# Optimization experiments

Hardware: AMD Instinct MI355X
Metric: run time of the kernel (lower is better)

The kernel has to match this reference:

```python
import jax, jax.numpy as jnp
import numpy as np

NUM_CODEBOOKS = 2
CODEBOOK_SIZE = 256
OUT_GROUP = 1
IN_GROUP = 8
IN_FEATURES = 4096
OUT_FEATURES = 11008


def setup_inputs() -> dict:
    key = jax.random.key(0)
    k1, k2, k3, k4, k5 = jax.random.split(key, 5)
    num_out_groups = OUT_FEATURES // OUT_GROUP
    num_in_groups = IN_FEATURES // IN_GROUP
    x = jax.random.normal(k1, (4, 2048, IN_FEATURES), dtype=jnp.float32)
    codes = jax.random.randint(k2, (num_out_groups, num_in_groups, NUM_CODEBOOKS), 0, CODEBOOK_SIZE, dtype=jnp.int32)
    codebooks = jax.random.normal(k3, (NUM_CODEBOOKS, CODEBOOK_SIZE, OUT_GROUP, IN_GROUP), dtype=jnp.float32) * 0.05
    scales = jax.random.uniform(k4, (num_out_groups, 1, 1, 1), dtype=jnp.float32)
    bias = jax.random.normal(k5, (OUT_FEATURES,), dtype=jnp.float32)
    return {"x": x, "codes": codes, "codebooks": codebooks, "scales": scales, "bias": bias}


def _dequantize_weight(codes, codebooks, scales):
    # codes: [Og, Ig, C] int; codebooks: [C, K, og, ig]; scales: [Og,1,1,1]
    C = codebooks.shape[0]
    og, ig = codebooks.shape[2], codebooks.shape[3]
    Og, Ig = codes.shape[0], codes.shape[1]
    # gather per-codebook vectors: result [Og, Ig, C, og, ig]
    w = codebooks[jnp.arange(C)[None, None, :], codes]
    w = w.sum(axis=2)                      # [Og, Ig, og, ig] (additive quantization)
    w = w * scales                         # broadcast [Og,1,1,1]
    w = w.transpose(0, 2, 1, 3)            # [Og, og, Ig, ig]
    return w.reshape(Og * og, Ig * ig)     # [out_features, in_features]


def reference(x, codes, codebooks, scales, bias):
    W = _dequantize_weight(codes, codebooks, scales)
    return jnp.einsum('bsi,oi->bso', x, W) + bias
```

## Files before the change

kernel.cpp:

```cpp
#include <hip/hip_runtime.h>
#include <hip/hip_bf16.h>
#include <stdint.h>

#define IN_F 4096
#define OUT_F 11008
#define M_ROWS 8192
#define NIG 512
#define CBSZ 256

typedef _Float16 f16x8 __attribute__((ext_vector_type(8)));
typedef float f32x4 __attribute__((ext_vector_type(4)));

__global__ __launch_bounds__(256) void dequant_w_kernel(
    const int* __restrict__ codes, const float* __restrict__ cbs,
    _Float16* __restrict__ W)
{
  const int idx = blockIdx.x * 256 + threadIdx.x;
  const int2 c = ((const int2*)codes)[idx];
  const float4* e0 = (const float4*)(cbs + (size_t)c.x * 8);
  const float4* e1 = (const float4*)(cbs + (size_t)CBSZ * 8 + (size_t)c.y * 8);
  const float4 a0 = e0[0], a1 = e0[1];
  const float4 b0 = e1[0], b1 = e1[1];
  f16x8 w;
  w[0] = (_Float16)(a0.x + b0.x);
  w[1] = (_Float16)(a0.y + b0.y);
  w[2] = (_Float16)(a0.z + b0.z);
  w[3] = (_Float16)(a0.w + b0.w);
  w[4] = (_Float16)(a1.x + b1.x);
  w[5] = (_Float16)(a1.y + b1.y);
  w[6] = (_Float16)(a1.z + b1.z);
  w[7] = (_Float16)(a1.w + b1.w);
  *(f16x8*)(W + (size_t)idx * 8) = w;
}

__global__ __launch_bounds__(256) void convert_x_kernel(
    const float* __restrict__ x, _Float16* __restrict__ X)
{
  const size_t i = ((size_t)blockIdx.x * 256 + threadIdx.x) * 8;
  const float4 a = *(const float4*)(x + i);
  const float4 b = *(const float4*)(x + i + 4);
  f16x8 v;
  v[0] = (_Float16)a.x; v[1] = (_Float16)a.y;
  v[2] = (_Float16)a.z; v[3] = (_Float16)a.w;
  v[4] = (_Float16)b.x; v[5] = (_Float16)b.y;
  v[6] = (_Float16)b.z; v[7] = (_Float16)b.w;
  *(f16x8*)(X + i) = v;
}

#define BM 256
#define BN 256
#define BK 64
#define NKT (IN_F / BK)
#define GRID_MT (M_ROWS / BM)
#define GRID_NT (OUT_F / BN)

__global__ __launch_bounds__(512, 2) void gemm_pipe(
    const _Float16* __restrict__ X, const _Float16* __restrict__ Wd,
    const float* __restrict__ scales, const float* __restrict__ bias,
    float* __restrict__ out)
{
  __shared__ char smem[131072];

  const int cpx = (GRID_MT * GRID_NT) >> 3;
  const int wg = (blockIdx.x & 7) * cpx + (blockIdx.x >> 3);
  const int mt = wg & (GRID_MT - 1), nt = wg >> 5;
  const int m0 = mt * BM, n0 = nt * BN;

  const int t_ = threadIdx.x;
  const int wave = t_ >> 6, lane = t_ & 63;
  const int wm = wave >> 2, wn = wave & 3;
  const int r16 = lane & 15;
  const int q = lane >> 4;
  const int sw = r16 & 7;
  const int c0 = ((q ^ sw) << 4);
  const int c1 = (((4 | q) ^ sw) << 4);

  const int s_row0 = t_ >> 3;
  const int s_col  = (((t_ & 7) ^ ((t_ >> 3) & 7)) << 3);
  const _Float16* asrc = X  + (size_t)(m0 + s_row0) * IN_F + s_col;
  const _Float16* bsrc = Wd + (size_t)(n0 + s_row0) * IN_F + s_col;
  const int s_dst = wave * 1024;

  f32x4 acc[8][4] = {};
  f16x8 al0[4], al1[4], ah0[4], ah1[4], bl0[2], bl1[2], bh0[2], bh1[2];

#define GLD(gsrc, ldst) __builtin_amdgcn_global_load_lds(                     \
    (const __attribute__((address_space(1))) void*)(gsrc),                    \
    (__attribute__((address_space(3))) void*)(ldst), 16, 0, 0)
#define STAGE_A(kt, bufc, i) GLD(asrc + (size_t)(kt) * BK + (size_t)(i) * 64 * IN_F, \
    smem + (bufc) * 65536 + (i) * 8192 + s_dst)
#define STAGE_B(kt, bufc, i) GLD(bsrc + (size_t)(kt) * BK + (size_t)(i) * 64 * IN_F, \
    smem + (bufc) * 65536 + 32768 + (i) * 8192 + s_dst)

#define RD_A(bufp, mm, cc) (*(const f16x8*)((bufp) + ((wm * 128 + (mm) * 16 + r16) << 7) + (cc)))
#define RD_B(bufp, nn, cc) (*(const f16x8*)((bufp) + 32768 + ((wn * 64 + (nn) * 16 + r16) << 7) + (cc)))

#define BAR   __builtin_amdgcn_s_barrier()
#define PRIO1 __builtin_amdgcn_s_setprio(1)
#define PRIO0 __builtin_amdgcn_s_setprio(0)
#define VM4 asm volatile("s_waitcnt vmcnt(4)" ::: "memory")
#define VM2 asm volatile("s_waitcnt vmcnt(2)" ::: "memory")
#define VM0 asm volatile("s_waitcnt vmcnt(0)" ::: "memory")

#define MG(AF, BF, MO, NO)                                                    \
    _Pragma("unroll")                                                         \
    for (int m = 0; m < 4; ++m)                                               \
      _Pragma("unroll")                                                       \
      for (int n = 0; n < 2; ++n)                                             \
        acc[(MO) + m][(NO) + n] = __builtin_amdgcn_mfma_f32_16x16x32_f16(     \
            AF[m], BF[n], acc[(MO) + m][(NO) + n], 0, 0, 0)

#define TILE(P, tt, STG, G2, G4) do {                                         \
    const char* bufT = smem + (P) * 65536;                                    \
                           \
    if (STG) { STAGE_A((tt) + 1, 1 - (P), 0); STAGE_A((tt) + 1, 1 - (P), 2); }\
    _Pragma("unroll")                                                         \
    for (int m = 0; m < 4; ++m) { al0[m] = RD_A(bufT, m, c0);                 \
                                  al1[m] = RD_A(bufT, m, c1); }               \
    _Pragma("unroll")                                                         \
    for (int n = 0; n < 2; ++n) { bl0[n] = RD_B(bufT, n, c0);                 \
                                  bl1[n] = RD_B(bufT, n, c1); }               \
    BAR; PRIO1; MG(al0, bl0, 0, 0); MG(al1, bl1, 0, 0); PRIO0; BAR;           \
                        \
    if (STG) { STAGE_B((tt) + 1, 1 - (P), 0); STAGE_B((tt) + 1, 1 - (P), 1); }\
    _Pragma("unroll")                                                         \
    for (int n = 0; n < 2; ++n) { bh0[n] = RD_B(bufT, 2 + n, c0);             \
                                  bh1[n] = RD_B(bufT, 2 + n, c1); }           \
    BAR; PRIO1; MG(al0, bh0, 0, 2); MG(al1, bh1, 0, 2); PRIO0;                \
    if ((G2) == 4) { VM4; }                                                   \
    if ((G2) == 0) { VM0; }                                                   \
    BAR;                                                                      \
                              \
    if (STG) { STAGE_B((tt) + 1, 1 - (P), 2); STAGE_B((tt) + 1, 1 - (P), 3); }\
    _Pragma("unroll")                                                         \
    for (int m = 0; m < 4; ++m) { ah0[m] = RD_A(bufT, 4 + m, c0);             \
                                  ah1[m] = RD_A(bufT, 4 + m, c1); }           \
    BAR; PRIO1; MG(ah0, bh0, 4, 2); MG(ah1, bh1, 4, 2); PRIO0; BAR;           \
                        \
    if (STG) { STAGE_A((tt) + 1, 1 - (P), 1); STAGE_A((tt) + 1, 1 - (P), 3); }\
    PRIO1; MG(ah0, bl0, 4, 0); MG(ah1, bl1, 4, 0); PRIO0;                     \
    if ((G4) == 2) { VM2; }                                                   \
    BAR;                                                                      \
  } while (0)

  STAGE_A(0, 0, 0); STAGE_A(0, 0, 2);
  STAGE_B(0, 0, 0); STAGE_B(0, 0, 1);
  STAGE_B(0, 0, 2); STAGE_B(0, 0, 3);
  STAGE_A(0, 0, 1); STAGE_A(0, 0, 3);
  VM2;
  BAR;

  #pragma unroll 1
  for (int t = 0; t < 62; t += 2) {
    TILE(0, t,     1, 4, 2);
    TILE(1, t + 1, 1, 4, 2);
  }
  TILE(0, 62, 1, 4, 2);
  TILE(1, 63, 0, 0, -1);

  const int crow = (lane >> 4) << 2;
  #pragma unroll
  for (int nf = 0; nf < 4; ++nf) {
    const int col = n0 + wn * 64 + nf * 16 + r16;
    const float s = scales[col];
    const float bb = bias[col];
    #pragma unroll
    for (int mf = 0; mf < 8; ++mf) {
      const int rb = m0 + wm * 128 + mf * 16 + crow;
      #pragma unroll
      for (int r = 0; r < 4; ++r)
        out[(size_t)(rb + r) * OUT_F + col] = acc[mf][nf][r] * s + bb;
    }
  }
#undef TILE
#undef MG
#undef RD_A
#undef RD_B
#undef STAGE_A
#undef STAGE_B
#undef GLD
}

__global__ __launch_bounds__(256) void naive_kernel(
    const float* __restrict__ x, const int* __restrict__ codes,
    const float* __restrict__ cbs, const float* __restrict__ scales,
    const float* __restrict__ bias, float* __restrict__ out)
{
  __shared__ float xrow[IN_F];
  const int m = blockIdx.x;
  for (int i = threadIdx.x; i < IN_F; i += 256)
    xrow[i] = x[(size_t)m * IN_F + i];
  __syncthreads();
  for (int o = threadIdx.x; o < OUT_F; o += 256) {
    float acc = 0.f;
    const int2* crow = (const int2*)codes + (size_t)o * NIG;
    for (int g = 0; g < NIG; ++g) {
      const int2 c = crow[g];
      const float* e0 = cbs + (size_t)c.x * 8;
      const float* e1 = cbs + (size_t)CBSZ * 8 + (size_t)c.y * 8;
      const float* xr = xrow + g * 8;
      #pragma unroll
      for (int j = 0; j < 8; ++j) acc += (e0[j] + e1[j]) * xr[j];
    }
    out[(size_t)m * OUT_F + o] = acc * scales[o] + bias[o];
  }
}

extern "C" void kernel_launch(void* const* d_in, const int* in_sizes, int n_in,
                              void* d_out, int out_size, void* d_ws, size_t ws_size,
                              hipStream_t stream) {
  const float* x      = (const float*)d_in[0];
  const int*   codes  = (const int*)d_in[1];
  const float* cbs    = (const float*)d_in[2];
  const float* scales = (const float*)d_in[3];
  const float* bias   = (const float*)d_in[4];
  float* out = (float*)d_out;

  const size_t W_BYTES = (size_t)OUT_F * IN_F * sizeof(_Float16);
  const size_t X_BYTES = (size_t)M_ROWS * IN_F * sizeof(_Float16);

  if (ws_size < W_BYTES + X_BYTES) {
    naive_kernel<<<M_ROWS, 256, 0, stream>>>(x, codes, cbs, scales, bias, out);
    return;
  }

  _Float16* W = (_Float16*)d_ws;
  _Float16* X = (_Float16*)((char*)d_ws + W_BYTES);

  dequant_w_kernel<<<(OUT_F * NIG) / 256, 256, 0, stream>>>(codes, cbs, W);
  convert_x_kernel<<<(M_ROWS * IN_F / 8) / 256, 256, 0, stream>>>(x, X);
  gemm_pipe<<<GRID_MT * GRID_NT, 512, 0, stream>>>(X, W, scales, bias, out);
}
```

Before: 818.0 us.

## Issue all next-tile loads up front and cut per-tile barriers to one

Restructures the double-buffered GEMM main loop so that all eight global-to-LDS loads for the next K tile are issued at the start of each tile, instead of being spread across four phases. The LDS reads and MFMAs are regrouped by K half (c0, then c1), and sched_barrier fences replace most workgroup barriers, leaving a single vmcnt(0) wait plus one barrier per tile. This is meant to cut barrier and synchronisation overhead and let MFMA issue run longer without stalls. In exchange, each tile ends with a full wait on outstanding loads, which removes the partial-wait overlap the old vmcnt(4)/vmcnt(2) schedule had and may expose load latency.

```diff
diff --git a/kernel.cpp b/kernel.cpp
--- a/kernel.cpp
+++ b/kernel.cpp
@@ -98,8 +98,7 @@
 #define BAR   __builtin_amdgcn_s_barrier()
 #define PRIO1 __builtin_amdgcn_s_setprio(1)
 #define PRIO0 __builtin_amdgcn_s_setprio(0)
-#define VM4 asm volatile("s_waitcnt vmcnt(4)" ::: "memory")
-#define VM2 asm volatile("s_waitcnt vmcnt(2)" ::: "memory")
+#define SBAR0 __builtin_amdgcn_sched_barrier(0)
 #define VM0 asm volatile("s_waitcnt vmcnt(0)" ::: "memory")
 
 #define MG(AF, BF, MO, NO)                                                    \
@@ -110,53 +109,58 @@
         acc[(MO) + m][(NO) + n] = __builtin_amdgcn_mfma_f32_16x16x32_f16(     \
             AF[m], BF[n], acc[(MO) + m][(NO) + n], 0, 0, 0)
 
-#define TILE(P, tt, STG, G2, G4) do {                                         \
+#define TILE(P, tt, STG, GATE) do {                                           \
     const char* bufT = smem + (P) * 65536;                                    \
-                           \
-    if (STG) { STAGE_A((tt) + 1, 1 - (P), 0); STAGE_A((tt) + 1, 1 - (P), 2); }\
-    _Pragma("unroll")                                                         \
-    for (int m = 0; m < 4; ++m) { al0[m] = RD_A(bufT, m, c0);                 \
-                                  al1[m] = RD_A(bufT, m, c1); }               \
+    if (STG) {                                                                \
+      STAGE_A((tt) + 1, 1 - (P), 0); STAGE_A((tt) + 1, 1 - (P), 1);           \
+      STAGE_A((tt) + 1, 1 - (P), 2); STAGE_A((tt) + 1, 1 - (P), 3);           \
+      STAGE_B((tt) + 1, 1 - (P), 0); STAGE_B((tt) + 1, 1 - (P), 1);           \
+      STAGE_B((tt) + 1, 1 - (P), 2); STAGE_B((tt) + 1, 1 - (P), 3);           \
+    }                                                                         \
+    SBAR0;                                                                    \
+         \
+    _Pragma("unroll")                                                         \
+    for (int m = 0; m < 4; ++m) al0[m] = RD_A(bufT, m, c0);                   \
     _Pragma("unroll")                                                         \
     for (int n = 0; n < 2; ++n) { bl0[n] = RD_B(bufT, n, c0);                 \
-                                  bl1[n] = RD_B(bufT, n, c1); }               \
-    BAR; PRIO1; MG(al0, bl0, 0, 0); MG(al1, bl1, 0, 0); PRIO0; BAR;           \
-                        \
-    if (STG) { STAGE_B((tt) + 1, 1 - (P), 0); STAGE_B((tt) + 1, 1 - (P), 1); }\
-    _Pragma("unroll")                                                         \
-    for (int n = 0; n < 2; ++n) { bh0[n] = RD_B(bufT, 2 + n, c0);             \
+                                  bh0[n] = RD_B(bufT, 2 + n, c0); }           \
+    _Pragma("unroll")                                                         \
+    for (int m = 0; m < 4; ++m) ah0[m] = RD_A(bufT, 4 + m, c0);               \
+    SBAR0;                                                                    \
+    PRIO1;                                                                    \
+    MG(al0, bl0, 0, 0); MG(al0, bh0, 0, 2);                                   \
+    MG(ah0, bh0, 4, 2); MG(ah0, bl0, 4, 0);                                   \
+    PRIO0;                                                                    \
+    SBAR0;                                                                    \
+                                                           \
+    _Pragma("unroll")                                                         \
+    for (int m = 0; m < 4; ++m) al1[m] = RD_A(bufT, m, c1);                   \
+    _Pragma("unroll")                                                         \
+    for (int n = 0; n < 2; ++n) { bl1[n] = RD_B(bufT, n, c1);                 \
                                   bh1[n] = RD_B(bufT, 2 + n, c1); }           \
-    BAR; PRIO1; MG(al0, bh0, 0, 2); MG(al1, bh1, 0, 2); PRIO0;                \
-    if ((G2) == 4) { VM4; }                                                   \
-    if ((G2) == 0) { VM0; }                                                   \
-    BAR;                                                                      \
-                              \
-    if (STG) { STAGE_B((tt) + 1, 1 - (P), 2); STAGE_B((tt) + 1, 1 - (P), 3); }\
-    _Pragma("unroll")                                                         \
-    for (int m = 0; m < 4; ++m) { ah0[m] = RD_A(bufT, 4 + m, c0);             \
-                                  ah1[m] = RD_A(bufT, 4 + m, c1); }           \
-    BAR; PRIO1; MG(ah0, bh0, 4, 2); MG(ah1, bh1, 4, 2); PRIO0; BAR;           \
-                        \
-    if (STG) { STAGE_A((tt) + 1, 1 - (P), 1); STAGE_A((tt) + 1, 1 - (P), 3); }\
-    PRIO1; MG(ah0, bl0, 4, 0); MG(ah1, bl1, 4, 0); PRIO0;                     \
-    if ((G4) == 2) { VM2; }                                                   \
-    BAR;                                                                      \
+    _Pragma("unroll")                                                         \
+    for (int m = 0; m < 4; ++m) ah1[m] = RD_A(bufT, 4 + m, c1);               \
+    SBAR0;                                                                    \
+    PRIO1;                                                                    \
+    MG(al1, bl1, 0, 0); MG(al1, bh1, 0, 2);                                   \
+    MG(ah1, bh1, 4, 2); MG(ah1, bl1, 4, 0);                                   \
+    PRIO0;                                                                    \
+    SBAR0;                                                                    \
+    if (GATE) { VM0; BAR; }       \
   } while (0)
 
-  STAGE_A(0, 0, 0); STAGE_A(0, 0, 2);
-  STAGE_B(0, 0, 0); STAGE_B(0, 0, 1);
-  STAGE_B(0, 0, 2); STAGE_B(0, 0, 3);
-  STAGE_A(0, 0, 1); STAGE_A(0, 0, 3);
-  VM2;
+  STAGE_A(0, 0, 0); STAGE_A(0, 0, 1); STAGE_A(0, 0, 2); STAGE_A(0, 0, 3);
+  STAGE_B(0, 0, 0); STAGE_B(0, 0, 1); STAGE_B(0, 0, 2); STAGE_B(0, 0, 3);
+  VM0;
   BAR;
 
   #pragma unroll 1
   for (int t = 0; t < 62; t += 2) {
-    TILE(0, t,     1, 4, 2);
-    TILE(1, t + 1, 1, 4, 2);
-  }
-  TILE(0, 62, 1, 4, 2);
-  TILE(1, 63, 0, 0, -1);
+    TILE(0, t,     1, 1);
+    TILE(1, t + 1, 1, 1);
+  }
+  TILE(0, 62, 1, 1);
+  TILE(1, 63, 0, 0);
 
   const int crow = (lane >> 4) << 2;
   #pragma unroll
```

Result: slower. 854.8 us (+4.5%).

## Load B operand straight from global into registers and drop its LDS staging

Applied to the files above, without the earlier changes.

The GEMM no longer stages the dequantized weight tile (B) through shared memory. Each wave now loads its B fragments directly from global memory into registers, prefetching the next k-tile's low half one tile ahead. Only the activation tile (A) stays double-buffered in LDS, which halves the LDS footprint. Most intra-tile workgroup barriers become scheduling barriers, with a single vmcnt wait plus barrier per tile. The aim is to cut LDS traffic and barrier stalls, at the cost of duplicated B global/L2 reads across the two M-waves and exposed global-load latency in registers.

```diff
diff --git a/kernel.cpp b/kernel.cpp
--- a/kernel.cpp
+++ b/kernel.cpp
@@ -59,7 +59,7 @@
     const float* __restrict__ scales, const float* __restrict__ bias,
     float* __restrict__ out)
 {
-  __shared__ char smem[131072];
+  __shared__ char smem[65536];
 
   const int cpx = (GRID_MT * GRID_NT) >> 3;
   const int wg = (blockIdx.x & 7) * cpx + (blockIdx.x >> 3);
@@ -77,30 +77,30 @@
 
   const int s_row0 = t_ >> 3;
   const int s_col  = (((t_ & 7) ^ ((t_ >> 3) & 7)) << 3);
-  const _Float16* asrc = X  + (size_t)(m0 + s_row0) * IN_F + s_col;
-  const _Float16* bsrc = Wd + (size_t)(n0 + s_row0) * IN_F + s_col;
+  const _Float16* asrc = X + (size_t)(m0 + s_row0) * IN_F + s_col;
   const int s_dst = wave * 1024;
 
+  const _Float16* bptr = Wd + (size_t)(n0 + wn * 64 + r16) * IN_F + q * 8;
+
   f32x4 acc[8][4] = {};
-  f16x8 al0[4], al1[4], ah0[4], ah1[4], bl0[2], bl1[2], bh0[2], bh1[2];
+  f16x8 af0[4], af1[4];
+  f16x8 bl0[2][2], bl1[2][2];
+  f16x8 bh0[2], bh1[2];
 
 #define GLD(gsrc, ldst) __builtin_amdgcn_global_load_lds(                     \
     (const __attribute__((address_space(1))) void*)(gsrc),                    \
     (__attribute__((address_space(3))) void*)(ldst), 16, 0, 0)
 #define STAGE_A(kt, bufc, i) GLD(asrc + (size_t)(kt) * BK + (size_t)(i) * 64 * IN_F, \
-    smem + (bufc) * 65536 + (i) * 8192 + s_dst)
-#define STAGE_B(kt, bufc, i) GLD(bsrc + (size_t)(kt) * BK + (size_t)(i) * 64 * IN_F, \
-    smem + (bufc) * 65536 + 32768 + (i) * 8192 + s_dst)
+    smem + (bufc) * 32768 + (i) * 8192 + s_dst)
 
 #define RD_A(bufp, mm, cc) (*(const f16x8*)((bufp) + ((wm * 128 + (mm) * 16 + r16) << 7) + (cc)))
-#define RD_B(bufp, nn, cc) (*(const f16x8*)((bufp) + 32768 + ((wn * 64 + (nn) * 16 + r16) << 7) + (cc)))
+#define LDB(dst, nf, hh, kt) dst = *(const f16x8*)(bptr + (size_t)(nf) * 16 * IN_F + (size_t)(kt) * BK + (hh) * 32)
 
 #define BAR   __builtin_amdgcn_s_barrier()
 #define PRIO1 __builtin_amdgcn_s_setprio(1)
 #define PRIO0 __builtin_amdgcn_s_setprio(0)
+#define SBAR0 __builtin_amdgcn_sched_barrier(0)
 #define VM4 asm volatile("s_waitcnt vmcnt(4)" ::: "memory")
-#define VM2 asm volatile("s_waitcnt vmcnt(2)" ::: "memory")
-#define VM0 asm volatile("s_waitcnt vmcnt(0)" ::: "memory")
 
 #define MG(AF, BF, MO, NO)                                                    \
     _Pragma("unroll")                                                         \
@@ -110,53 +110,51 @@
         acc[(MO) + m][(NO) + n] = __builtin_amdgcn_mfma_f32_16x16x32_f16(     \
             AF[m], BF[n], acc[(MO) + m][(NO) + n], 0, 0, 0)
 
-#define TILE(P, tt, STG, G2, G4) do {                                         \
-    const char* bufT = smem + (P) * 65536;                                    \
-                           \
-    if (STG) { STAGE_A((tt) + 1, 1 - (P), 0); STAGE_A((tt) + 1, 1 - (P), 2); }\
-    _Pragma("unroll")                                                         \
-    for (int m = 0; m < 4; ++m) { al0[m] = RD_A(bufT, m, c0);                 \
-                                  al1[m] = RD_A(bufT, m, c1); }               \
-    _Pragma("unroll")                                                         \
-    for (int n = 0; n < 2; ++n) { bl0[n] = RD_B(bufT, n, c0);                 \
-                                  bl1[n] = RD_B(bufT, n, c1); }               \
-    BAR; PRIO1; MG(al0, bl0, 0, 0); MG(al1, bl1, 0, 0); PRIO0; BAR;           \
-                        \
-    if (STG) { STAGE_B((tt) + 1, 1 - (P), 0); STAGE_B((tt) + 1, 1 - (P), 1); }\
-    _Pragma("unroll")                                                         \
-    for (int n = 0; n < 2; ++n) { bh0[n] = RD_B(bufT, 2 + n, c0);             \
-                                  bh1[n] = RD_B(bufT, 2 + n, c1); }           \
-    BAR; PRIO1; MG(al0, bh0, 0, 2); MG(al1, bh1, 0, 2); PRIO0;                \
-    if ((G2) == 4) { VM4; }                                                   \
-    if ((G2) == 0) { VM0; }                                                   \
-    BAR;                                                                      \
-                              \
-    if (STG) { STAGE_B((tt) + 1, 1 - (P), 2); STAGE_B((tt) + 1, 1 - (P), 3); }\
-    _Pragma("unroll")                                                         \
-    for (int m = 0; m < 4; ++m) { ah0[m] = RD_A(bufT, 4 + m, c0);             \
-                                  ah1[m] = RD_A(bufT, 4 + m, c1); }           \
-    BAR; PRIO1; MG(ah0, bh0, 4, 2); MG(ah1, bh1, 4, 2); PRIO0; BAR;           \
-                        \
-    if (STG) { STAGE_A((tt) + 1, 1 - (P), 1); STAGE_A((tt) + 1, 1 - (P), 3); }\
-    PRIO1; MG(ah0, bl0, 4, 0); MG(ah1, bl1, 4, 0); PRIO0;                     \
-    if ((G4) == 2) { VM2; }                                                   \
-    BAR;                                                                      \
+#define TILE(P, tt, STG, LBL, GATE) do {                                      \
+    const char* Ab = smem + (P) * 32768;                                      \
+                   \
+    if (STG) { STAGE_A((tt) + 1, 1 - (P), 0); STAGE_A((tt) + 1, 1 - (P), 1); }\
+    _Pragma("unroll")                                                         \
+    for (int m = 0; m < 4; ++m) { af0[m] = RD_A(Ab, m, c0);                   \
+                                  af1[m] = RD_A(Ab, m, c1); }                 \
+    _Pragma("unroll")                                                         \
+    for (int n = 0; n < 2; ++n) { LDB(bh0[n], 2 + n, 0, tt);                  \
+                                  LDB(bh1[n], 2 + n, 1, tt); }                \
+    SBAR0; PRIO1; MG(af0, bl0[P], 0, 0); MG(af1, bl1[P], 0, 0); PRIO0; SBAR0; \
+                                           \
+    if (STG) { STAGE_A((tt) + 1, 1 - (P), 2); STAGE_A((tt) + 1, 1 - (P), 3); }\
+    SBAR0; PRIO1; MG(af0, bh0, 0, 2); MG(af1, bh1, 0, 2); PRIO0; SBAR0;       \
+       \
+    _Pragma("unroll")                                                         \
+    for (int m = 0; m < 4; ++m) { af0[m] = RD_A(Ab, 4 + m, c0);               \
+                                  af1[m] = RD_A(Ab, 4 + m, c1); }             \
+    if (LBL) {                                                                \
+      _Pragma("unroll")                                                       \
+      for (int n = 0; n < 2; ++n) { LDB(bl0[1 - (P)][n], n, 0, (tt) + 1);     \
+                                    LDB(bl1[1 - (P)][n], n, 1, (tt) + 1); }   \
+    }                                                                         \
+    SBAR0; PRIO1; MG(af0, bh0, 4, 2); MG(af1, bh1, 4, 2); PRIO0; SBAR0;       \
+                             \
+    PRIO1; MG(af0, bl0[P], 4, 0); MG(af1, bl1[P], 4, 0); PRIO0; SBAR0;        \
+    if (GATE) { VM4; BAR; }                                                   \
   } while (0)
 
-  STAGE_A(0, 0, 0); STAGE_A(0, 0, 2);
-  STAGE_B(0, 0, 0); STAGE_B(0, 0, 1);
-  STAGE_B(0, 0, 2); STAGE_B(0, 0, 3);
-  STAGE_A(0, 0, 1); STAGE_A(0, 0, 3);
-  VM2;
+  STAGE_A(0, 0, 0); STAGE_A(0, 0, 1); STAGE_A(0, 0, 2); STAGE_A(0, 0, 3);
+  {
+    _Pragma("unroll")
+    for (int n = 0; n < 2; ++n) { LDB(bl0[0][n], n, 0, 0);
+                                  LDB(bl1[0][n], n, 1, 0); }
+  }
+  VM4;
   BAR;
 
   #pragma unroll 1
   for (int t = 0; t < 62; t += 2) {
-    TILE(0, t,     1, 4, 2);
-    TILE(1, t + 1, 1, 4, 2);
-  }
-  TILE(0, 62, 1, 4, 2);
-  TILE(1, 63, 0, 0, -1);
+    TILE(0, t,     1, 1, 1);
+    TILE(1, t + 1, 1, 1, 1);
+  }
+  TILE(0, 62, 1, 1, 1);
+  TILE(1, 63, 0, 0, 0);
 
   const int crow = (lane >> 4) << 2;
   #pragma unroll
@@ -175,9 +173,8 @@
 #undef TILE
 #undef MG
 #undef RD_A
-#undef RD_B
+#undef LDB
 #undef STAGE_A
-#undef STAGE_B
 #undef GLD
 }
 
```

Measured after the change: 1.084 ms. 32.5% more time.

## Switch GEMM to 32x32x16 MFMA and prefetch B two tiles ahead

Applied to the files above, without the earlier changes.

Replaces the 16x16x32 MFMA tiling with 32x32x16 MFMA fragments and reorganizes the per-tile schedule into four k-slices. Each slice reloads A while B fragments are held across the whole tile. B staging now targets tile t+2 into the current buffer once it has been consumed, and A staging targets t+1, which changes the prefetch depth and the waitcnt gating. The aim is to cut LDS reads per MFMA and raise MFMA efficiency. In exchange, the pipeline ordering and the vmcnt accounting become riskier.

```diff
diff --git a/kernel.cpp b/kernel.cpp
--- a/kernel.cpp
+++ b/kernel.cpp
@@ -10,6 +10,7 @@
 
 typedef _Float16 f16x8 __attribute__((ext_vector_type(8)));
 typedef float f32x4 __attribute__((ext_vector_type(4)));
+typedef float f32x16 __attribute__((ext_vector_type(16)));
 
 __global__ __launch_bounds__(256) void dequant_w_kernel(
     const int* __restrict__ codes, const float* __restrict__ cbs,
@@ -69,11 +70,13 @@
   const int t_ = threadIdx.x;
   const int wave = t_ >> 6, lane = t_ & 63;
   const int wm = wave >> 2, wn = wave & 3;
-  const int r16 = lane & 15;
-  const int q = lane >> 4;
-  const int sw = r16 & 7;
-  const int c0 = ((q ^ sw) << 4);
-  const int c1 = (((4 | q) ^ sw) << 4);
+  const int r32 = lane & 31;
+  const int q2 = lane >> 5;
+  const int sw = lane & 7;
+  const int ck0 = (((0 + q2) ^ sw) << 4);
+  const int ck1 = (((2 + q2) ^ sw) << 4);
+  const int ck2 = (((4 + q2) ^ sw) << 4);
+  const int ck3 = (((6 + q2) ^ sw) << 4);
 
   const int s_row0 = t_ >> 3;
   const int s_col  = (((t_ & 7) ^ ((t_ >> 3) & 7)) << 3);
@@ -81,8 +84,9 @@
   const _Float16* bsrc = Wd + (size_t)(n0 + s_row0) * IN_F + s_col;
   const int s_dst = wave * 1024;
 
-  f32x4 acc[8][4] = {};
-  f16x8 al0[4], al1[4], ah0[4], ah1[4], bl0[2], bl1[2], bh0[2], bh1[2];
+  f32x16 acc[4][2] = {};
+  f16x8 a[4];
+  f16x8 b[2][4];
 
 #define GLD(gsrc, ldst) __builtin_amdgcn_global_load_lds(                     \
     (const __attribute__((address_space(1))) void*)(gsrc),                    \
@@ -92,84 +96,82 @@
 #define STAGE_B(kt, bufc, i) GLD(bsrc + (size_t)(kt) * BK + (size_t)(i) * 64 * IN_F, \
     smem + (bufc) * 65536 + 32768 + (i) * 8192 + s_dst)
 
-#define RD_A(bufp, mm, cc) (*(const f16x8*)((bufp) + ((wm * 128 + (mm) * 16 + r16) << 7) + (cc)))
-#define RD_B(bufp, nn, cc) (*(const f16x8*)((bufp) + 32768 + ((wn * 64 + (nn) * 16 + r16) << 7) + (cc)))
+#define RD_A(bufp, mf, cc) (*(const f16x8*)((bufp) + ((wm * 128 + (mf) * 32 + r32) << 7) + (cc)))
+#define RD_B(bufp, nf, cc) (*(const f16x8*)((bufp) + 32768 + ((wn * 64 + (nf) * 32 + r32) << 7) + (cc)))
 
 #define BAR   __builtin_amdgcn_s_barrier()
 #define PRIO1 __builtin_amdgcn_s_setprio(1)
 #define PRIO0 __builtin_amdgcn_s_setprio(0)
 #define VM4 asm volatile("s_waitcnt vmcnt(4)" ::: "memory")
-#define VM2 asm volatile("s_waitcnt vmcnt(2)" ::: "memory")
 #define VM0 asm volatile("s_waitcnt vmcnt(0)" ::: "memory")
 
-#define MG(AF, BF, MO, NO)                                                    \
-    _Pragma("unroll")                                                         \
-    for (int m = 0; m < 4; ++m)                                               \
+#define MG(ks)                                                                \
+    _Pragma("unroll")                                                         \
+    for (int mf = 0; mf < 4; ++mf)                                            \
       _Pragma("unroll")                                                       \
-      for (int n = 0; n < 2; ++n)                                             \
-        acc[(MO) + m][(NO) + n] = __builtin_amdgcn_mfma_f32_16x16x32_f16(     \
-            AF[m], BF[n], acc[(MO) + m][(NO) + n], 0, 0, 0)
-
-#define TILE(P, tt, STG, G2, G4) do {                                         \
+      for (int nf = 0; nf < 2; ++nf)                                          \
+        acc[mf][nf] = __builtin_amdgcn_mfma_f32_32x32x16_f16(                 \
+            a[mf], b[nf][ks], acc[mf][nf], 0, 0, 0)
+
+#define TILE(P, tt, SA, SB, GATE) do {                                        \
     const char* bufT = smem + (P) * 65536;                                    \
-                           \
-    if (STG) { STAGE_A((tt) + 1, 1 - (P), 0); STAGE_A((tt) + 1, 1 - (P), 2); }\
-    _Pragma("unroll")                                                         \
-    for (int m = 0; m < 4; ++m) { al0[m] = RD_A(bufT, m, c0);                 \
-                                  al1[m] = RD_A(bufT, m, c1); }               \
-    _Pragma("unroll")                                                         \
-    for (int n = 0; n < 2; ++n) { bl0[n] = RD_B(bufT, n, c0);                 \
-                                  bl1[n] = RD_B(bufT, n, c1); }               \
-    BAR; PRIO1; MG(al0, bl0, 0, 0); MG(al1, bl1, 0, 0); PRIO0; BAR;           \
-                        \
-    if (STG) { STAGE_B((tt) + 1, 1 - (P), 0); STAGE_B((tt) + 1, 1 - (P), 1); }\
-    _Pragma("unroll")                                                         \
-    for (int n = 0; n < 2; ++n) { bh0[n] = RD_B(bufT, 2 + n, c0);             \
-                                  bh1[n] = RD_B(bufT, 2 + n, c1); }           \
-    BAR; PRIO1; MG(al0, bh0, 0, 2); MG(al1, bh1, 0, 2); PRIO0;                \
-    if ((G2) == 4) { VM4; }                                                   \
-    if ((G2) == 0) { VM0; }                                                   \
-    BAR;                                                                      \
                               \
-    if (STG) { STAGE_B((tt) + 1, 1 - (P), 2); STAGE_B((tt) + 1, 1 - (P), 3); }\
-    _Pragma("unroll")                                                         \
-    for (int m = 0; m < 4; ++m) { ah0[m] = RD_A(bufT, 4 + m, c0);             \
-                                  ah1[m] = RD_A(bufT, 4 + m, c1); }           \
-    BAR; PRIO1; MG(ah0, bh0, 4, 2); MG(ah1, bh1, 4, 2); PRIO0; BAR;           \
-                        \
-    if (STG) { STAGE_A((tt) + 1, 1 - (P), 1); STAGE_A((tt) + 1, 1 - (P), 3); }\
-    PRIO1; MG(ah0, bl0, 4, 0); MG(ah1, bl1, 4, 0); PRIO0;                     \
-    if ((G4) == 2) { VM2; }                                                   \
+    if (SA) { STAGE_A((tt) + 1, 1 - (P), 0); STAGE_A((tt) + 1, 1 - (P), 1); } \
+    _Pragma("unroll")                                                         \
+    for (int nf = 0; nf < 2; ++nf) {                                          \
+      b[nf][0] = RD_B(bufT, nf, ck0); b[nf][1] = RD_B(bufT, nf, ck1);         \
+      b[nf][2] = RD_B(bufT, nf, ck2); b[nf][3] = RD_B(bufT, nf, ck3);         \
+    }                                                                         \
+    _Pragma("unroll")                                                         \
+    for (int mf = 0; mf < 4; ++mf) a[mf] = RD_A(bufT, mf, ck0);               \
+    PRIO1; MG(0); PRIO0; BAR;                                                 \
+                                        \
+    if (SA) { STAGE_A((tt) + 1, 1 - (P), 2); STAGE_A((tt) + 1, 1 - (P), 3); } \
+    _Pragma("unroll")                                                         \
+    for (int mf = 0; mf < 4; ++mf) a[mf] = RD_A(bufT, mf, ck1);               \
+    PRIO1; MG(1); PRIO0; BAR;                                                 \
+       \
+    if (SB) { STAGE_B((tt) + 2, P, 0); STAGE_B((tt) + 2, P, 1); }             \
+    _Pragma("unroll")                                                         \
+    for (int mf = 0; mf < 4; ++mf) a[mf] = RD_A(bufT, mf, ck2);               \
+    PRIO1; MG(2); PRIO0; BAR;                                                 \
+                    \
+    if (SB) { STAGE_B((tt) + 2, P, 2); STAGE_B((tt) + 2, P, 3); }             \
+    _Pragma("unroll")                                                         \
+    for (int mf = 0; mf < 4; ++mf) a[mf] = RD_A(bufT, mf, ck3);               \
+    PRIO1; MG(3); PRIO0;                                                      \
+    if ((GATE) == 4) { VM4; }                                                 \
+    if ((GATE) == 0) { VM0; }                                                 \
     BAR;                                                                      \
   } while (0)
 
-  STAGE_A(0, 0, 0); STAGE_A(0, 0, 2);
-  STAGE_B(0, 0, 0); STAGE_B(0, 0, 1);
-  STAGE_B(0, 0, 2); STAGE_B(0, 0, 3);
-  STAGE_A(0, 0, 1); STAGE_A(0, 0, 3);
-  VM2;
+  STAGE_A(0, 0, 0); STAGE_A(0, 0, 1); STAGE_A(0, 0, 2); STAGE_A(0, 0, 3);
+  STAGE_B(0, 0, 0); STAGE_B(0, 0, 1); STAGE_B(0, 0, 2); STAGE_B(0, 0, 3);
+  STAGE_B(1, 1, 0); STAGE_B(1, 1, 1); STAGE_B(1, 1, 2); STAGE_B(1, 1, 3);
+  VM4;
   BAR;
 
   #pragma unroll 1
   for (int t = 0; t < 62; t += 2) {
-    TILE(0, t,     1, 4, 2);
-    TILE(1, t + 1, 1, 4, 2);
-  }
-  TILE(0, 62, 1, 4, 2);
+    TILE(0, t,     1, 1, 4);
+    TILE(1, t + 1, 1, 1, 4);
+  }
+  TILE(0, 62, 1, 0, 0);
   TILE(1, 63, 0, 0, -1);
 
-  const int crow = (lane >> 4) << 2;
   #pragma unroll
-  for (int nf = 0; nf < 4; ++nf) {
-    const int col = n0 + wn * 64 + nf * 16 + r16;
+  for (int nf = 0; nf < 2; ++nf) {
+    const int col = n0 + wn * 64 + nf * 32 + r32;
     const float s = scales[col];
     const float bb = bias[col];
     #pragma unroll
-    for (int mf = 0; mf < 8; ++mf) {
-      const int rb = m0 + wm * 128 + mf * 16 + crow;
+    for (int mf = 0; mf < 4; ++mf) {
+      const int rb = m0 + wm * 128 + mf * 32 + 4 * q2;
       #pragma unroll
-      for (int r = 0; r < 4; ++r)
-        out[(size_t)(rb + r) * OUT_F + col] = acc[mf][nf][r] * s + bb;
+      for (int reg = 0; reg < 16; ++reg) {
+        const int row = rb + (reg & 3) + 8 * (reg >> 2);
+        out[(size_t)row * OUT_F + col] = acc[mf][nf][reg] * s + bb;
+      }
     }
   }
 #undef TILE
```

After: 809.6 us. Within noise of the previous version (-1.0%).
